# Optimization experiments

Hardware: AMD Instinct MI355X
Metric: run time of the kernel (lower is better)

Reference implementation:

```python
import jax, jax.numpy as jnp
import numpy as np
import math
from jax import lax

B, HS, WS, C, T, TD, HH, TOPM = 8, 64, 64, 512, 77, 512, 8, 3
DH = C // HH
CONF_TH = 0.35


def _layernorm(x, w, b, eps=1e-5):
    mu = x.mean(-1, keepdims=True)
    var = ((x - mu) ** 2).mean(-1, keepdims=True)
    return (x - mu) * lax.rsqrt(var + eps) * w + b


def _l2norm(x, eps=1e-6):
    n = jnp.sqrt((x * x).sum(-1, keepdims=True))
    return x / jnp.maximum(n, eps)


def _forward(visual_features, text_features, geo_mask,
             ln1_w, ln1_b, wq, bq, wk, bk, wv, bv, wo, bo,
             gate_w, gate_b, logit_scale, alpha,
             ln2_w, ln2_b, ffn_w1, ffn_b1, ffn_w2, ffn_b2):
    Bb, Hs, Ws, Cv = visual_features.shape
    N = Hs * Ws
    # Pre-LN + flatten spatial
    x = _layernorm(visual_features, ln1_w, ln1_b).reshape(Bb, N, Cv)
    q_full = x @ wq + bq                                  # [B,N,C]
    pad_mask = jnp.abs(text_features).sum(-1) <= 1e-6     # [B,T]
    k_full = text_features @ wk + bk                      # [B,T,C]
    v_full = text_features @ wv + bv
    # per-token L2 normalize over full channel dim, then split heads
    q = _l2norm(q_full).reshape(Bb, N, HH, DH)
    k = _l2norm(k_full).reshape(Bb, T, HH, DH)
    v = v_full.reshape(Bb, T, HH, DH)
    scale = jnp.exp(jnp.clip(logit_scale, -2.0, 2.0)) / jnp.sqrt(jnp.float32(DH))
    sim = jnp.einsum('bnhd,bthd->bnht', q, k) * scale     # [B,N,H,T]
    # geo gate (4D tensor branch): log-bias on logits + multiplicative channel gate later
    gate_map = jnp.clip(geo_mask, 0.3, 1.0)               # [B,1,Hs,Ws]
    geo_gate_flat = gate_map.reshape(Bb, N, 1)            # [B,N,1]
    sim = sim + jnp.log(jnp.maximum(gate_map.reshape(Bb, N), 1e-6))[:, :, None, None]
    sim = jnp.where(pad_mask[:, None, None, :], -jnp.inf, sim)
    # Top-K sparsification before softmax (threshold at the K-th value)
    topv = lax.top_k(sim, TOPM)[0]                        # [B,N,H,K]
    sim = jnp.where(sim >= topv[..., -1:], sim, -jnp.inf)
    attn = jax.nn.softmax(sim, axis=-1)
    attn = attn / jnp.maximum(attn.sum(-1, keepdims=True), 1e-6)
    # fully-padded rows -> zero
    all_pad = pad_mask.all(axis=1)
    attn = jnp.where(all_pad[:, None, None, None], 0.0, attn)
    # confidence bypass: conf = max_prob * (1 - normalized entropy), mean over heads
    a_hn = attn.transpose(0, 2, 1, 3)                     # [B,H,N,T]
    maxp = a_hn.max(-1, keepdims=True)
    t_eff = jnp.maximum((a_hn > 0).astype(a_hn.dtype).sum(-1, keepdims=True), 2.0)
    p = jnp.maximum(a_hn, 1e-8)
    ent = jnp.maximum(-(p * jnp.log(p)).sum(-1, keepdims=True) / jnp.log(t_eff), 0.0)
    conf = jnp.clip(maxp * (1.0 - ent), 0.0, 1.0).mean(axis=1)   # [B,N,1]
    conf_scale = CONF_TH + (1.0 - CONF_TH) * jnp.clip(conf, 0.0, 1.0)
    aligned = jnp.einsum('bnht,bthd->bnhd', attn, v).reshape(Bb, N, HH * DH)
    aligned = (aligned @ wo + bo) * conf_scale
    gate = jax.nn.sigmoid(x @ gate_w + gate_b) * geo_gate_flat
    y = x + alpha * gate * aligned
    h = _layernorm(y, ln2_w, ln2_b)
    y = y + (jax.nn.gelu(h @ ffn_w1 + ffn_b1, approximate=False) @ ffn_w2 + ffn_b2)
    return y.reshape(Bb, Hs, Ws, Cv)


def setup_inputs() -> dict:
    key = jax.random.key(0)
    ks = jax.random.split(key, 16)
    def w(k, shp, fan_in):
        return (jax.random.normal(k, shp, jnp.float32) * (1.0 / math.sqrt(fan_in))).astype(jnp.float32)
    return {
        'visual_features': jax.random.normal(ks[0], (B, HS, WS, C), jnp.float32),
        'text_features':   jax.random.normal(ks[1], (B, T, TD), jnp.float32),
        'geo_mask':        jax.random.uniform(ks[2], (B, 1, HS, WS), jnp.float32),
        'ln1_w': jnp.ones((C,), jnp.float32), 'ln1_b': jnp.zeros((C,), jnp.float32),
        'wq': w(ks[3], (C, C), C),   'bq': jnp.zeros((C,), jnp.float32),
        'wk': w(ks[4], (TD, C), TD), 'bk': jnp.zeros((C,), jnp.float32),
        'wv': w(ks[5], (TD, C), TD), 'bv': jnp.zeros((C,), jnp.float32),
        'wo': w(ks[6], (C, C), C),   'bo': jnp.zeros((C,), jnp.float32),
        'gate_w': w(ks[7], (C, C), C), 'gate_b': jnp.zeros((C,), jnp.float32),
        'logit_scale': jnp.float32(math.log(1.0 / 0.07)),
        'alpha': jnp.float32(0.1),
        'ln2_w': jnp.ones((C,), jnp.float32), 'ln2_b': jnp.zeros((C,), jnp.float32),
        'ffn_w1': w(ks[8], (C, 4 * C), C),    'ffn_b1': jnp.zeros((4 * C,), jnp.float32),
        'ffn_w2': w(ks[9], (4 * C, C), 4 * C), 'ffn_b2': jnp.zeros((C,), jnp.float32),
    }


def reference(visual_features, text_features, geo_mask,
              ln1_w, ln1_b, wq, bq, wk, bk, wv, bv, wo, bo,
              gate_w, gate_b, logit_scale, alpha,
              ln2_w, ln2_b, ffn_w1, ffn_b1, ffn_w2, ffn_b2):
    return _forward(visual_features, text_features, geo_mask,
                    ln1_w, ln1_b, wq, bq, wk, bk, wv, bv, wo, bo,
                    gate_w, gate_b, logit_scale, alpha,
                    ln2_w, ln2_b, ffn_w1, ffn_b1, ffn_w2, ffn_b2)
```

## Files before the change

kernel.cpp:

```cpp
#include <hip/hip_runtime.h>
#include <hip/hip_bf16.h>
#include <math.h>

#define TT 77
#define MTOT 32768

typedef __attribute__((ext_vector_type(8))) short bf16x8;
typedef __attribute__((ext_vector_type(4))) float floatx4;

#define GPTR(p) ((const __attribute__((address_space(1))) void*)(p))
#define LPTR(p) ((__attribute__((address_space(3))) void*)(p))

__device__ __forceinline__ float wred_sum(float v) {
#pragma unroll
  for (int o = 32; o >= 1; o >>= 1) v += __shfl_xor(v, o, 64);
  return v;
}

__device__ __forceinline__ unsigned short f2bf(float f) {
  unsigned int u = __float_as_uint(f);
  unsigned int r = (u + 0x7fffu + ((u >> 16) & 1u)) >> 16;
  return (unsigned short)r;
}
__device__ __forceinline__ float bf2f(unsigned short h) {
  return __uint_as_float(((unsigned int)h) << 16);
}
__device__ __forceinline__ unsigned int cvt2bf(float a, float b) {
  unsigned int r;
  asm("v_cvt_pk_bf16_f32 %0, %1, %2" : "=v"(r) : "v"(a), "v"(b));
  return r;
}

__device__ __forceinline__ float fast_gelu(float o) {
  const float z = fabsf(o) * 0.70710678118654752f;
  const float t = __builtin_amdgcn_rcpf(fmaf(0.3275911f, z, 1.0f));
  float p = fmaf(1.061405429f, t, -1.453152027f);
  p = fmaf(p, t, 1.421413741f);
  p = fmaf(p, t, -0.284496736f);
  p = fmaf(p, t, 0.254829592f);
  p = p * t;
  const float erfz = fmaf(-p, __expf(-z * z), 1.0f);
  const float s = __builtin_copysignf(erfz, o);
  return 0.5f * o * (1.0f + s);
}

__device__ __forceinline__ float fast_sigmoid(float o) {
  return __builtin_amdgcn_rcpf(1.0f + __expf(-o));
}

__global__ __launch_bounds__(256)
void ln_bf16_kernel(const float* __restrict__ in, const float* __restrict__ gw,
                    const float* __restrict__ gb, unsigned short* __restrict__ out) {
  const int wv = threadIdx.x >> 6, lane = threadIdx.x & 63;
  const size_t row = (size_t)blockIdx.x * 4 + wv;
  const float* p = in + row * 512 + lane * 8;
  float4 a = *(const float4*)p;
  float4 b = *(const float4*)(p + 4);
  float s = a.x + a.y + a.z + a.w + b.x + b.y + b.z + b.w;
  float mu = wred_sum(s) * (1.0f / 512.0f);
  float d[8] = {a.x - mu, a.y - mu, a.z - mu, a.w - mu,
                b.x - mu, b.y - mu, b.z - mu, b.w - mu};
  float ss = 0.f;
#pragma unroll
  for (int i = 0; i < 8; ++i) ss = fmaf(d[i], d[i], ss);
  float var = wred_sum(ss) * (1.0f / 512.0f);
  float rstd = rsqrtf(var + 1e-5f);
  float4 w0 = *(const float4*)(gw + lane * 8);
  float4 w1 = *(const float4*)(gw + lane * 8 + 4);
  float4 c0 = *(const float4*)(gb + lane * 8);
  float4 c1 = *(const float4*)(gb + lane * 8 + 4);
  float o[8];
  o[0] = d[0] * rstd * w0.x + c0.x;  o[1] = d[1] * rstd * w0.y + c0.y;
  o[2] = d[2] * rstd * w0.z + c0.z;  o[3] = d[3] * rstd * w0.w + c0.w;
  o[4] = d[4] * rstd * w1.x + c1.x;  o[5] = d[5] * rstd * w1.y + c1.y;
  o[6] = d[6] * rstd * w1.z + c1.z;  o[7] = d[7] * rstd * w1.w + c1.w;
  __align__(16) unsigned short ob[8];
#pragma unroll
  for (int i = 0; i < 8; ++i) ob[i] = f2bf(o[i]);
  *(uint4*)(out + row * 512 + lane * 8) = *(const uint4*)ob;
}

__global__ __launch_bounds__(256)
void zero_acc_kernel(float* __restrict__ ssq, float* __restrict__ conf) {
  const int i = blockIdx.x * 256 + threadIdx.x;
  ssq[i] = 0.0f;
  conf[i] = 0.0f;
}

__global__ __launch_bounds__(256)
void transpose_bf16_kernel(const float* __restrict__ W, unsigned short* __restrict__ WTb,
                           int K, int N) {
  __shared__ float s[32][33];
  const int tx = threadIdx.x & 31, ty = threadIdx.x >> 5;
  const int n0 = blockIdx.x * 32, k0 = blockIdx.y * 32;
#pragma unroll
  for (int j = 0; j < 4; ++j)
    s[ty + 8 * j][tx] = W[(size_t)(k0 + ty + 8 * j) * N + n0 + tx];
  __syncthreads();
#pragma unroll
  for (int j = 0; j < 4; ++j)
    WTb[(size_t)(n0 + ty + 8 * j) * K + k0 + tx] = f2bf(s[tx][ty + 8 * j]);
}

__global__ __launch_bounds__(256)
void transpose_pair_kernel(const float* __restrict__ W,
                           unsigned short* __restrict__ WTh,
                           unsigned short* __restrict__ WTl, int K, int N) {
  __shared__ float s[32][33];
  const int tx = threadIdx.x & 31, ty = threadIdx.x >> 5;
  const int n0 = blockIdx.x * 32, k0 = blockIdx.y * 32;
#pragma unroll
  for (int j = 0; j < 4; ++j)
    s[ty + 8 * j][tx] = W[(size_t)(k0 + ty + 8 * j) * N + n0 + tx];
  __syncthreads();
#pragma unroll
  for (int j = 0; j < 4; ++j) {
    const float a = s[tx][ty + 8 * j];
    const unsigned short hi = f2bf(a);
    WTh[(size_t)(n0 + ty + 8 * j) * K + k0 + tx] = hi;
    WTl[(size_t)(n0 + ty + 8 * j) * K + k0 + tx] = f2bf(a - bf2f(hi));
  }
}

__global__ __launch_bounds__(256)
void text_cvt_kernel(const float* __restrict__ text,
                     unsigned short* __restrict__ thi,
                     unsigned short* __restrict__ tlo,
                     float* __restrict__ negm) {
  const int wv = threadIdx.x >> 6, lane = threadIdx.x & 63;
  const int row = blockIdx.x * 4 + wv;
  if (row >= 616) {
    const uint4 z = {0u, 0u, 0u, 0u};
    *(uint4*)(thi + (size_t)row * 512 + lane * 8) = z;
    *(uint4*)(tlo + (size_t)row * 512 + lane * 8) = z;
    return;
  }
  const float* p = text + (size_t)row * 512 + lane * 8;
  float4 a = *(const float4*)p;
  float4 b = *(const float4*)(p + 4);
  float v[8] = {a.x, a.y, a.z, a.w, b.x, b.y, b.z, b.w};
  float ab = 0.f;
#pragma unroll
  for (int i = 0; i < 8; ++i) ab += fabsf(v[i]);
  ab = wred_sum(ab);
  __align__(16) unsigned short hb[8];
  __align__(16) unsigned short lb[8];
#pragma unroll
  for (int i = 0; i < 8; ++i) {
    hb[i] = f2bf(v[i]);
    lb[i] = f2bf(v[i] - bf2f(hb[i]));
  }
  *(uint4*)(thi + (size_t)row * 512 + lane * 8) = *(const uint4*)hb;
  *(uint4*)(tlo + (size_t)row * 512 + lane * 8) = *(const uint4*)lb;
  if (lane == 0) {
    const int bb = row / 77, t = row - bb * 77;
    negm[bb * 80 + t] = (ab <= 1e-6f) ? -INFINITY : 0.0f;
  }
}

__global__ __launch_bounds__(256)
void kv_gemm(const unsigned short* __restrict__ AH,
             const unsigned short* __restrict__ AL,
             const unsigned short* __restrict__ BH,
             const unsigned short* __restrict__ BL,
             const float* __restrict__ bk, const float* __restrict__ bv,
             float* __restrict__ outp) {
  const int K = 512;
  __shared__ __align__(16) unsigned short AsH[128 * 32];
  __shared__ __align__(16) unsigned short AsL[128 * 32];
  __shared__ __align__(16) unsigned short BsH[128 * 32];
  __shared__ __align__(16) unsigned short BsL[128 * 32];
  const int tid = threadIdx.x;
  const int wid = tid >> 6, lane = tid & 63;
  const int wr = wid >> 1, wc = wid & 1;
  const int m16 = lane & 15, quad = lane >> 4;
  const int row0 = blockIdx.y * 128, col0 = blockIdx.x * 128;

  const floatx4 zero4 = {0.f, 0.f, 0.f, 0.f};
  floatx4 acc[4][4];
#pragma unroll
  for (int i = 0; i < 4; ++i)
#pragma unroll
    for (int j = 0; j < 4; ++j) acc[i][j] = zero4;

  const int srow = tid >> 2;
  const int schunk = (tid & 3) ^ (srow & 3);
  const unsigned short* AgH = AH + (size_t)(row0 + srow) * K + schunk * 8;
  const unsigned short* AgL = AL + (size_t)(row0 + srow) * K + schunk * 8;
  const unsigned short* BgH = BH + (size_t)(col0 + srow) * K + schunk * 8;
  const unsigned short* BgL = BL + (size_t)(col0 + srow) * K + schunk * 8;
  char* AsHB = (char*)AsH + tid * 16;
  char* AsLB = (char*)AsL + tid * 16;
  char* BsHB = (char*)BsH + tid * 16;
  char* BsLB = (char*)BsL + tid * 16;
  const int rq = quad ^ (m16 & 3);
  const int aOfs = (wr * 64 + m16) * 32 + rq * 8;
  const int bOfs = (wc * 64 + m16) * 32 + rq * 8;

  for (int k0 = 0; k0 < K; k0 += 32) {
    __syncthreads();
    __builtin_amdgcn_global_load_lds(GPTR(AgH + k0), LPTR(AsHB), 16, 0, 0);
    __builtin_amdgcn_global_load_lds(GPTR(AgH + (size_t)64 * K + k0), LPTR(AsHB + 4096), 16, 0, 0);
    __builtin_amdgcn_global_load_lds(GPTR(AgL + k0), LPTR(AsLB), 16, 0, 0);
    __builtin_amdgcn_global_load_lds(GPTR(AgL + (size_t)64 * K + k0), LPTR(AsLB + 4096), 16, 0, 0);
    __builtin_amdgcn_global_load_lds(GPTR(BgH + k0), LPTR(BsHB), 16, 0, 0);
    __builtin_amdgcn_global_load_lds(GPTR(BgH + (size_t)64 * K + k0), LPTR(BsHB + 4096), 16, 0, 0);
    __builtin_amdgcn_global_load_lds(GPTR(BgL + k0), LPTR(BsLB), 16, 0, 0);
    __builtin_amdgcn_global_load_lds(GPTR(BgL + (size_t)64 * K + k0), LPTR(BsLB + 4096), 16, 0, 0);
    __syncthreads();
    bf16x8 afH[4], afL[4], bfH[4], bfL[4];
#pragma unroll
    for (int i = 0; i < 4; ++i) {
      afH[i] = *(const bf16x8*)(AsH + aOfs + i * 16 * 32);
      afL[i] = *(const bf16x8*)(AsL + aOfs + i * 16 * 32);
      bfH[i] = *(const bf16x8*)(BsH + bOfs + i * 16 * 32);
      bfL[i] = *(const bf16x8*)(BsL + bOfs + i * 16 * 32);
    }
#pragma unroll
    for (int mi = 0; mi < 4; ++mi)
#pragma unroll
      for (int ni = 0; ni < 4; ++ni) {
        acc[mi][ni] = __builtin_amdgcn_mfma_f32_16x16x32_bf16(afH[mi], bfH[ni], acc[mi][ni], 0, 0, 0);
        acc[mi][ni] = __builtin_amdgcn_mfma_f32_16x16x32_bf16(afH[mi], bfL[ni], acc[mi][ni], 0, 0, 0);
        acc[mi][ni] = __builtin_amdgcn_mfma_f32_16x16x32_bf16(afL[mi], bfH[ni], acc[mi][ni], 0, 0, 0);
      }
  }

  const float* bp = (col0 < 512) ? bk : bv;
  const int cbase = (col0 < 512) ? col0 : col0 - 512;
  float bb[4];
#pragma unroll
  for (int ni = 0; ni < 4; ++ni) bb[ni] = bp[cbase + wc * 64 + ni * 16 + m16];
#pragma unroll
  for (int mi = 0; mi < 4; ++mi)
#pragma unroll
    for (int r = 0; r < 4; ++r) {
      const int row = row0 + wr * 64 + mi * 16 + quad * 4 + r;
#pragma unroll
      for (int ni = 0; ni < 4; ++ni) {
        const int col = col0 + wc * 64 + ni * 16 + m16;
        outp[(size_t)row * 1024 + col] = acc[mi][ni][r] + bb[ni];
      }
    }
}

__global__ __launch_bounds__(256)
void knorm_kernel(const float* __restrict__ KV,
                  unsigned short* __restrict__ khb) {
  const int wv = threadIdx.x >> 6, lane = threadIdx.x & 63;
  const int row = blockIdx.x * 4 + wv;
  const float* p = KV + (size_t)row * 1024 + lane * 8;
  float4 a = *(const float4*)p;
  float4 b = *(const float4*)(p + 4);
  float v[8] = {a.x, a.y, a.z, a.w, b.x, b.y, b.z, b.w};
  float ss = 0.f;
#pragma unroll
  for (int i = 0; i < 8; ++i) ss = fmaf(v[i], v[i], ss);
  ss = wred_sum(ss);
  const float sc = 1.0f / fmaxf(sqrtf(ss), 1e-6f);
  const int bb = row / 77, t = row - bb * 77;
  const int c = lane * 8, h = c >> 6, d = c & 63;
  __align__(16) unsigned short ob[8];
#pragma unroll
  for (int i = 0; i < 8; ++i) ob[i] = f2bf(v[i] * sc);
  *(uint4*)(khb + (((size_t)bb * 8 + h) * 80 + t) * 64 + d) = *(const uint4*)ob;
}

__global__ __launch_bounds__(256)
void kpad_zero_kernel(unsigned short* __restrict__ khb, float* __restrict__ negm) {
  const int i = blockIdx.x * 256 + threadIdx.x;
  const int bh = i / 192, rem = i - bh * 192;
  const int t = 77 + rem / 64, d = rem & 63;
  khb[(((size_t)bh) * 80 + t) * 64 + d] = 0;
  if (i < 24) negm[(i / 3) * 80 + 77 + (i % 3)] = -INFINITY;
}

__global__ __launch_bounds__(256)
void sim_attn_kernel(const unsigned short* __restrict__ qnb,
                     const unsigned short* __restrict__ khb,
                     const float* __restrict__ negm,
                     const float* __restrict__ ssq,
                     const float* __restrict__ logit_scale,
                     const float* __restrict__ vf,
                     unsigned short* __restrict__ alignedb,
                     float* __restrict__ confacc) {
  __shared__ __align__(16) char lbuf[128 * 81 * 4];
  unsigned short* As = (unsigned short*)lbuf;
  unsigned short* Bs = As + 128 * 72;
  float* simt = (float*)lbuf;

  const int bh = blockIdx.y;
  const int b = bh >> 3, h = bh & 7;
  const int row0 = blockIdx.x * 128;
  const int tid = threadIdx.x;

  {
    const int r = tid >> 1, half = tid & 1;
    const unsigned short* src = qnb + ((size_t)b * 4096 + row0 + r) * 512 + h * 64 + half * 32;
    unsigned short* dst = As + r * 72 + half * 32;
    *(uint4*)dst = *(const uint4*)src;
    *(uint4*)(dst + 8) = *(const uint4*)(src + 8);
    *(uint4*)(dst + 16) = *(const uint4*)(src + 16);
    *(uint4*)(dst + 24) = *(const uint4*)(src + 24);
  }
  if (tid < 160) {
    const int r = tid >> 1, half = tid & 1;
    const unsigned short* src = khb + ((size_t)bh * 80 + r) * 64 + half * 32;
    unsigned short* dst = Bs + r * 72 + half * 32;
    *(uint4*)dst = *(const uint4*)src;
    *(uint4*)(dst + 8) = *(const uint4*)(src + 8);
    *(uint4*)(dst + 16) = *(const uint4*)(src + 16);
    *(uint4*)(dst + 24) = *(const uint4*)(src + 24);
  }
  __syncthreads();

  const int w = tid >> 6, lane = tid & 63;
  const int m16 = lane & 15, quad = lane >> 4;
  const unsigned short* aBase = As + (w * 32 + m16) * 72 + quad * 8;
  const unsigned short* bBase = Bs + m16 * 72 + quad * 8;
  bf16x8 af[2][2], bf[5][2];
#pragma unroll
  for (int mi = 0; mi < 2; ++mi)
#pragma unroll
    for (int kk = 0; kk < 2; ++kk)
      af[mi][kk] = *(const bf16x8*)(aBase + mi * 16 * 72 + kk * 32);
#pragma unroll
  for (int ni = 0; ni < 5; ++ni)
#pragma unroll
    for (int kk = 0; kk < 2; ++kk)
      bf[ni][kk] = *(const bf16x8*)(bBase + ni * 16 * 72 + kk * 32);
  __syncthreads();

  const floatx4 zero4 = {0.f, 0.f, 0.f, 0.f};
  floatx4 acc[2][5];
#pragma unroll
  for (int mi = 0; mi < 2; ++mi)
#pragma unroll
    for (int ni = 0; ni < 5; ++ni) acc[mi][ni] = zero4;
#pragma unroll
  for (int kk = 0; kk < 2; ++kk)
#pragma unroll
    for (int mi = 0; mi < 2; ++mi)
#pragma unroll
      for (int ni = 0; ni < 5; ++ni)
        acc[mi][ni] = __builtin_amdgcn_mfma_f32_16x16x32_bf16(af[mi][kk], bf[ni][kk], acc[mi][ni], 0, 0, 0);

  const float ls = fminf(fmaxf(logit_scale[0], -2.0f), 2.0f);
  const float scale = expf(ls) * 0.125f;
  float nm[5];
#pragma unroll
  for (int ni = 0; ni < 5; ++ni) nm[ni] = negm[b * 80 + ni * 16 + m16];
#pragma unroll
  for (int mi = 0; mi < 2; ++mi)
#pragma unroll
    for (int r = 0; r < 4; ++r) {
      const int lr = w * 32 + quad * 4 + mi * 16 + r;
      const float ssv = ssq[(size_t)b * 4096 + row0 + lr];
      const float nsc = scale / fmaxf(sqrtf(ssv), 1e-6f);
#pragma unroll
      for (int ni = 0; ni < 5; ++ni)
        simt[lr * 81 + ni * 16 + m16] = acc[mi][ni][r] * nsc + nm[ni];
    }
  __syncthreads();

  const int lr = tid >> 1, half = tid & 1;
  const int n = row0 + lr;
  const float* sp = simt + lr * 81;

  float m1 = -INFINITY, m2 = -INFINITY, m3 = -INFINITY, m4 = -INFINITY;
  int a1 = 0, a2 = 0, a3 = 0;
  for (int t = 0; t < 80; ++t) {
    const float v = sp[t];
    const bool c1 = v > m1, c2 = v > m2, c3 = v > m3, c4 = v > m4;
    m4 = c4 ? (c3 ? m3 : v) : m4;
    m3 = c3 ? (c2 ? m2 : v) : m3;
    a3 = c3 ? (c2 ? a2 : t) : a3;
    m2 = c2 ? (c1 ? m1 : v) : m2;
    a2 = c2 ? (c1 ? a1 : t) : a2;
    m1 = c1 ? v : m1;
    a1 = c1 ? t : a1;
  }

  const bool dead = (m1 == -INFINITY);
  if (dead) m1 = 0.0f;
  const bool tie = (!dead) && ((m1 == m2) || (m2 == m3) || (m3 == m4));

  const float d2 = m2 - m1, d3 = m3 - m1;
  const float e2 = __expf(d2), e3 = __expf(d3);
  float s0 = 1.0f + e2 + e3;
  float s1 = ((e2 > 0.f) ? e2 * d2 : 0.f) + ((e3 > 0.f) ? e3 * d3 : 0.f);
  float cntf = 1.0f + ((e2 > 0.f) ? 1.f : 0.f) + ((e3 > 0.f) ? 1.f : 0.f);

  unsigned short* op = alignedb + ((size_t)b * 4096 + n) * 512 + h * 64 + half * 32;

  if (tie) {
    s0 = 0.f; s1 = 0.f; cntf = 0.f;
    float4 acc2[8];
#pragma unroll
    for (int i = 0; i < 8; ++i) acc2[i] = (float4){0.f, 0.f, 0.f, 0.f};
    for (int t = 0; t < 80; ++t) {
      const float v = sp[t];
      if (v >= m3) {
        const float e = expf(v - m1);
        if (e > 0.f) {
          s0 += e; s1 = fmaf(e, v - m1, s1); cntf += 1.f;
          const float4* vp = (const float4*)(vf + (size_t)(b * 77 + t) * 1024 + h * 64 + half * 32);
#pragma unroll
          for (int i = 0; i < 8; ++i) {
            const float4 x = vp[i];
            acc2[i].x = fmaf(e, x.x, acc2[i].x);
            acc2[i].y = fmaf(e, x.y, acc2[i].y);
            acc2[i].z = fmaf(e, x.z, acc2[i].z);
            acc2[i].w = fmaf(e, x.w, acc2[i].w);
          }
        }
      }
    }
    const float invt = 1.0f / s0;
#pragma unroll
    for (int i = 0; i < 4; ++i) {
      const float4 lo = acc2[2 * i], hi = acc2[2 * i + 1];
      uint4 pk;
      pk.x = cvt2bf(lo.x * invt, lo.y * invt);
      pk.y = cvt2bf(lo.z * invt, lo.w * invt);
      pk.z = cvt2bf(hi.x * invt, hi.y * invt);
      pk.w = cvt2bf(hi.z * invt, hi.w * invt);
      *(uint4*)(op + i * 8) = pk;
    }
  } else {
    const float inv0 = 1.0f / s0;
    const float wA = dead ? 0.f : inv0;
    const float wB = e2 * inv0, wC = e3 * inv0;
    const float* v1p = vf + (size_t)(b * 77 + a1) * 1024 + h * 64 + half * 32;
    const float* v2p = vf + (size_t)(b * 77 + a2) * 1024 + h * 64 + half * 32;
    const float* v3p = vf + (size_t)(b * 77 + a3) * 1024 + h * 64 + half * 32;
#pragma unroll
    for (int i = 0; i < 4; ++i) {
      const float4 x0 = ((const float4*)v1p)[2 * i];
      const float4 x1 = ((const float4*)v1p)[2 * i + 1];
      const float4 y0 = ((const float4*)v2p)[2 * i];
      const float4 y1 = ((const float4*)v2p)[2 * i + 1];
      const float4 z0 = ((const float4*)v3p)[2 * i];
      const float4 z1 = ((const float4*)v3p)[2 * i + 1];
      float4 r0, r1;
      r0.x = fmaf(wC, z0.x, fmaf(wB, y0.x, wA * x0.x));
      r0.y = fmaf(wC, z0.y, fmaf(wB, y0.y, wA * x0.y));
      r0.z = fmaf(wC, z0.z, fmaf(wB, y0.z, wA * x0.z));
      r0.w = fmaf(wC, z0.w, fmaf(wB, y0.w, wA * x0.w));
      r1.x = fmaf(wC, z1.x, fmaf(wB, y1.x, wA * x1.x));
      r1.y = fmaf(wC, z1.y, fmaf(wB, y1.y, wA * x1.y));
      r1.z = fmaf(wC, z1.z, fmaf(wB, y1.z, wA * x1.z));
      r1.w = fmaf(wC, z1.w, fmaf(wB, y1.w, wA * x1.w));
      uint4 pk;
      pk.x = cvt2bf(r0.x, r0.y);
      pk.y = cvt2bf(r0.z, r0.w);
      pk.z = cvt2bf(r1.x, r1.y);
      pk.w = cvt2bf(r1.z, r1.w);
      *(uint4*)(op + i * 8) = pk;
    }
  }

  if (half == 0) {
    const float inv = 1.0f / s0;
    const float entn = (__logf(s0) - s1 * inv) + (77.0f - cntf) * 1.8420681e-7f;
    const float ent = fmaxf(entn / __logf(fmaxf(cntf, 2.0f)), 0.0f);
    float conf_h = fminf(fmaxf(inv * (1.0f - ent), 0.0f), 1.0f);
    if (dead) conf_h = 0.f;
    atomicAdd(confacc + (size_t)b * 4096 + n, conf_h * 0.125f);
  }
}

template <int EPI, int KC>
__global__ __launch_bounds__(256)
void mfma_gemm(const unsigned short* __restrict__ A,
               const unsigned short* __restrict__ WT,
               const float* __restrict__ bias,
               void* __restrict__ outv, int M, int N,
               const unsigned short* __restrict__ e0b,
               const float* __restrict__ e1f,
               const float* __restrict__ e2f,
               const float* __restrict__ scf) {
  __shared__ __align__(16) unsigned short As[128 * 64];
  __shared__ __align__(16) unsigned short Bs[128 * 64];
  const int tid = threadIdx.x;
  const int wid = tid >> 6, lane = tid & 63;
  const int wr = wid >> 1, wc = wid & 1;
  const int m16 = lane & 15, quad = lane >> 4;

  const int nwg = gridDim.x * gridDim.y;
  const int orig = blockIdx.y * gridDim.x + blockIdx.x;
  const int qq = nwg >> 3, rr = nwg & 7;
  const int xcd = orig & 7, base = orig >> 3;
  const int logical = (xcd < rr ? xcd * (qq + 1) : rr * (qq + 1) + (xcd - rr) * qq) + base;
  const int bx = logical % gridDim.x, by = logical / gridDim.x;
  const int row0 = by * 128, col0 = bx * 128;

  const floatx4 zero4 = {0.f, 0.f, 0.f, 0.f};
  floatx4 acc[4][4];
#pragma unroll
  for (int i = 0; i < 4; ++i)
#pragma unroll
    for (int j = 0; j < 4; ++j) acc[i][j] = zero4;

  size_t aoff[4], boff[4];
  char* ldst[4];
#pragma unroll
  for (int j = 0; j < 4; ++j) {
    const int s = wid * 64 + j * 256 + lane;
    const int r = s >> 3;
    const int gc = (s & 7) ^ (r & 7);
    aoff[j] = (size_t)(row0 + r) * KC + gc * 8;
    const int br = (r & 64) + 4 * (r & 15) + ((r >> 4) & 3);
    boff[j] = (size_t)(col0 + br) * KC + gc * 8;
    ldst[j] = (char*)nullptr + (size_t)s * 16;
  }

  for (int k0 = 0; k0 < KC; k0 += 64) {
    __syncthreads();
#pragma unroll
    for (int j = 0; j < 4; ++j) {
      __builtin_amdgcn_global_load_lds(GPTR(A + aoff[j] + k0), LPTR((char*)As + (size_t)(ldst[j] - (char*)nullptr)), 16, 0, 0);
      __builtin_amdgcn_global_load_lds(GPTR(WT + boff[j] + k0), LPTR((char*)Bs + (size_t)(ldst[j] - (char*)nullptr)), 16, 0, 0);
    }
    __syncthreads();
#pragma unroll
    for (int kk = 0; kk < 2; ++kk) {
      const int pc = (kk * 4 + quad) ^ (m16 & 7);
      bf16x8 af[4], bfr[4];
#pragma unroll
      for (int i = 0; i < 4; ++i) {
        af[i] = *(const bf16x8*)((const char*)As + (wr * 64 + i * 16 + m16) * 128 + pc * 16);
        bfr[i] = *(const bf16x8*)((const char*)Bs + (wc * 64 + i * 16 + m16) * 128 + pc * 16);
      }
#pragma unroll
      for (int mi = 0; mi < 4; ++mi)
#pragma unroll
        for (int ni = 0; ni < 4; ++ni)
          acc[mi][ni] = __builtin_amdgcn_mfma_f32_16x16x32_bf16(af[mi], bfr[ni], acc[mi][ni], 0, 0, 0);
    }
  }

  float* outf = (float*)outv;
  unsigned short* outb = (unsigned short*)outv;
  const unsigned short* albf = (const unsigned short*)e1f;
  const int colb = col0 + wc * 64 + 4 * m16;
  const float4 bbv = *(const float4*)(bias + colb);
  const float bb[4] = {bbv.x, bbv.y, bbv.z, bbv.w};
  const float alphav = (EPI == 2) ? scf[0] : 0.f;

#pragma unroll
  for (int mi = 0; mi < 4; ++mi) {
#pragma unroll
    for (int r = 0; r < 4; ++r) {
      const int row = row0 + wr * 64 + mi * 16 + quad * 4 + r;
      float o[4];
#pragma unroll
      for (int ni = 0; ni < 4; ++ni) o[ni] = acc[mi][ni][r] + bb[ni];
      const size_t basei = (size_t)row * N + colb;

      if (EPI == 5) {
        uint2 pk;
        pk.x = cvt2bf(o[0], o[1]);
        pk.y = cvt2bf(o[2], o[3]);
        *(uint2*)(outb + basei) = pk;
        float p = fmaf(o[0], o[0], fmaf(o[1], o[1], fmaf(o[2], o[2], o[3] * o[3])));
        p += __shfl_xor(p, 1, 64);
        p += __shfl_xor(p, 2, 64);
        p += __shfl_xor(p, 4, 64);
        p += __shfl_xor(p, 8, 64);
        if (m16 == 0) atomicAdd(const_cast<float*>(e1f) + row, p);
      } else if (EPI == 3) {
        uint2 pk;
        pk.x = cvt2bf(fast_gelu(o[0]), fast_gelu(o[1]));
        pk.y = cvt2bf(fast_gelu(o[2]), fast_gelu(o[3]));
        *(uint2*)(outb + basei) = pk;
      } else if (EPI == 1) {
        const float cm = fminf(fmaxf(e1f[row], 0.0f), 1.0f);
        const float rowscale = 0.35f + 0.65f * cm;
        uint2 pk;
        pk.x = cvt2bf(o[0] * rowscale, o[1] * rowscale);
        pk.y = cvt2bf(o[2] * rowscale, o[3] * rowscale);
        *(uint2*)(outb + basei) = pk;
      } else if (EPI == 2) {
        const float geo = fminf(fmaxf(e2f[row], 0.3f), 1.0f);
        const uint2 xpk = *(const uint2*)(e0b + basei);
        const uint2 apk = *(const uint2*)(albf + basei);
        const float xv[4] = {bf2f((unsigned short)xpk.x), bf2f((unsigned short)(xpk.x >> 16)),
                             bf2f((unsigned short)xpk.y), bf2f((unsigned short)(xpk.y >> 16))};
        const float av[4] = {bf2f((unsigned short)apk.x), bf2f((unsigned short)(apk.x >> 16)),
                             bf2f((unsigned short)apk.y), bf2f((unsigned short)(apk.y >> 16))};
        float4 ov;
        ov.x = xv[0] + alphav * fast_sigmoid(o[0]) * geo * av[0];
        ov.y = xv[1] + alphav * fast_sigmoid(o[1]) * geo * av[1];
        ov.z = xv[2] + alphav * fast_sigmoid(o[2]) * geo * av[2];
        ov.w = xv[3] + alphav * fast_sigmoid(o[3]) * geo * av[3];
        *(float4*)(outf + basei) = ov;
      } else {
        const float4 rv = *(const float4*)(e1f + basei);
        float4 ov;
        ov.x = o[0] + rv.x;
        ov.y = o[1] + rv.y;
        ov.z = o[2] + rv.z;
        ov.w = o[3] + rv.w;
        *(float4*)(outf + basei) = ov;
      }
    }
  }
}

extern "C" void kernel_launch(void* const* d_in, const int* in_sizes, int n_in,
                              void* d_out, int out_size, void* d_ws, size_t ws_size,
                              hipStream_t stream) {
  const float* visual = (const float*)d_in[0];
  const float* text   = (const float*)d_in[1];
  const float* geo    = (const float*)d_in[2];
  const float* ln1_w  = (const float*)d_in[3];
  const float* ln1_b  = (const float*)d_in[4];
  const float* wq     = (const float*)d_in[5];
  const float* bq     = (const float*)d_in[6];
  const float* wk     = (const float*)d_in[7];
  const float* bk     = (const float*)d_in[8];
  const float* wvw    = (const float*)d_in[9];
  const float* bv     = (const float*)d_in[10];
  const float* wo     = (const float*)d_in[11];
  const float* bo     = (const float*)d_in[12];
  const float* gate_w = (const float*)d_in[13];
  const float* gate_b = (const float*)d_in[14];
  const float* logit_scale = (const float*)d_in[15];
  const float* alpha  = (const float*)d_in[16];
  const float* ln2_w  = (const float*)d_in[17];
  const float* ln2_b  = (const float*)d_in[18];
  const float* ffn_w1 = (const float*)d_in[19];
  const float* ffn_b1 = (const float*)d_in[20];
  const float* ffn_w2 = (const float*)d_in[21];
  const float* ffn_b2 = (const float*)d_in[22];
  float* out = (float*)d_out;

  char* ws = (char*)d_ws;
  float* R0            = (float*)ws;
  float* BUF2          = (float*)(ws + 88080384);
  unsigned short* Xb   = (unsigned short*)(ws + 155189248);
  unsigned short* QNb  = (unsigned short*)(ws + 188743680);
  unsigned short* wqT  = (unsigned short*)(ws + 222298112);
  unsigned short* woT  = wqT + 262144;
  unsigned short* gateT = woT + 262144;
  unsigned short* w1T  = gateT + 262144;
  unsigned short* w2T  = w1T + 1048576;
  unsigned short* KHb  = w2T + 1048576;
  float* NEGM = (float*)(ws + 230146048);
  float* CONF = (float*)(ws + 230148608);
  float* SSQ  = (float*)(ws + 230279680);

  float* KV            = (float*)(ws + 88080384);
  unsigned short* THi  = (unsigned short*)(ws + 88080384 + 2621440);
  unsigned short* TLo  = THi + 640 * 512;
  unsigned short* WKVh = TLo + 640 * 512;
  unsigned short* WKVl = WKVh + 1024 * 512;

  unsigned short* ALb = (unsigned short*)R0;
  unsigned short* AOb = QNb;

  transpose_bf16_kernel<<<dim3(16, 16), 256, 0, stream>>>(wq, wqT, 512, 512);
  transpose_bf16_kernel<<<dim3(16, 16), 256, 0, stream>>>(wo, woT, 512, 512);
  transpose_bf16_kernel<<<dim3(16, 16), 256, 0, stream>>>(gate_w, gateT, 512, 512);
  transpose_bf16_kernel<<<dim3(64, 16), 256, 0, stream>>>(ffn_w1, w1T, 512, 2048);
  transpose_bf16_kernel<<<dim3(16, 64), 256, 0, stream>>>(ffn_w2, w2T, 2048, 512);
  transpose_pair_kernel<<<dim3(16, 16), 256, 0, stream>>>(wk, WKVh, WKVl, 512, 512);
  transpose_pair_kernel<<<dim3(16, 16), 256, 0, stream>>>(wvw, WKVh + 512 * 512, WKVl + 512 * 512, 512, 512);

  ln_bf16_kernel<<<MTOT / 4, 256, 0, stream>>>(visual, ln1_w, ln1_b, Xb);
  zero_acc_kernel<<<128, 256, 0, stream>>>(SSQ, CONF);
  text_cvt_kernel<<<160, 256, 0, stream>>>(text, THi, TLo, NEGM);
  kv_gemm<<<dim3(8, 5), 256, 0, stream>>>(THi, TLo, WKVh, WKVl, bk, bv, KV);
  knorm_kernel<<<154, 256, 0, stream>>>(KV, KHb);
  kpad_zero_kernel<<<48, 256, 0, stream>>>(KHb, NEGM);
  mfma_gemm<5, 512><<<dim3(4, 256), 256, 0, stream>>>(Xb, wqT, bq, QNb, MTOT, 512,
                                                      nullptr, SSQ, nullptr, nullptr);
  sim_attn_kernel<<<dim3(32, 64), 256, 0, stream>>>(QNb, KHb, NEGM, SSQ, logit_scale,
                                                    KV + 512, ALb, CONF);
  mfma_gemm<1, 512><<<dim3(4, 256), 256, 0, stream>>>(ALb, woT, bo, AOb, MTOT, 512,
                                                      nullptr, CONF, nullptr, nullptr);
  mfma_gemm<2, 512><<<dim3(4, 256), 256, 0, stream>>>(Xb, gateT, gate_b, BUF2, MTOT, 512,
                                                      Xb, (const float*)AOb, geo, alpha);
  ln_bf16_kernel<<<MTOT / 4, 256, 0, stream>>>(BUF2, ln2_w, ln2_b, Xb);
  unsigned short* GCH = (unsigned short*)R0;
  for (int ch = 0; ch < 2; ++ch) {
    const size_t off = (size_t)ch * 16384;
    mfma_gemm<3, 512><<<dim3(16, 128), 256, 0, stream>>>(Xb + off * 512, w1T, ffn_b1, GCH,
                                                         16384, 2048,
                                                         nullptr, nullptr, nullptr, nullptr);
    mfma_gemm<4, 2048><<<dim3(4, 128), 256, 0, stream>>>(GCH, w2T, ffn_b2, out + off * 512,
                                                         16384, 512,
                                                         nullptr, BUF2 + off * 512, nullptr, nullptr);
  }
}
```

Measured before the change: 567.6 us.

## Double-buffer LDS tiles in MFMA GEMM to overlap global loads with compute

```diff
diff --git a/kernel.cpp b/kernel.cpp
--- a/kernel.cpp
+++ b/kernel.cpp
@@ -480,8 +480,8 @@
                const float* __restrict__ e1f,
                const float* __restrict__ e2f,
                const float* __restrict__ scf) {
-  __shared__ __align__(16) unsigned short As[128 * 64];
-  __shared__ __align__(16) unsigned short Bs[128 * 64];
+  __shared__ __align__(16) unsigned short As[2][128 * 64];
+  __shared__ __align__(16) unsigned short Bs[2][128 * 64];
   const int tid = threadIdx.x;
   const int wid = tid >> 6, lane = tid & 63;
   const int wr = wid >> 1, wc = wid & 1;
@@ -503,7 +503,7 @@
     for (int j = 0; j < 4; ++j) acc[i][j] = zero4;
 
   size_t aoff[4], boff[4];
-  char* ldst[4];
+  unsigned int ldso[4];
 #pragma unroll
   for (int j = 0; j < 4; ++j) {
     const int s = wid * 64 + j * 256 + lane;
@@ -512,31 +512,45 @@
     aoff[j] = (size_t)(row0 + r) * KC + gc * 8;
     const int br = (r & 64) + 4 * (r & 15) + ((r >> 4) & 3);
     boff[j] = (size_t)(col0 + br) * KC + gc * 8;
-    ldst[j] = (char*)nullptr + (size_t)s * 16;
-  }
-
-  for (int k0 = 0; k0 < KC; k0 += 64) {
-    __syncthreads();
-#pragma unroll
-    for (int j = 0; j < 4; ++j) {
-      __builtin_amdgcn_global_load_lds(GPTR(A + aoff[j] + k0), LPTR((char*)As + (size_t)(ldst[j] - (char*)nullptr)), 16, 0, 0);
-      __builtin_amdgcn_global_load_lds(GPTR(WT + boff[j] + k0), LPTR((char*)Bs + (size_t)(ldst[j] - (char*)nullptr)), 16, 0, 0);
-    }
-    __syncthreads();
+    ldso[j] = (unsigned int)s * 16;
+  }
+
+  constexpr int NT = KC / 64;
+#pragma unroll
+  for (int j = 0; j < 4; ++j) {
+    __builtin_amdgcn_global_load_lds(GPTR(A + aoff[j]), LPTR((char*)As[0] + ldso[j]), 16, 0, 0);
+    __builtin_amdgcn_global_load_lds(GPTR(WT + boff[j]), LPTR((char*)Bs[0] + ldso[j]), 16, 0, 0);
+  }
+  __syncthreads();
+
+  int cur = 0;
+  for (int t = 0; t < NT; ++t) {
+    if (t + 1 < NT) {
+      const size_t k0n = (size_t)(t + 1) * 64;
+#pragma unroll
+      for (int j = 0; j < 4; ++j) {
+        __builtin_amdgcn_global_load_lds(GPTR(A + aoff[j] + k0n), LPTR((char*)As[cur ^ 1] + ldso[j]), 16, 0, 0);
+        __builtin_amdgcn_global_load_lds(GPTR(WT + boff[j] + k0n), LPTR((char*)Bs[cur ^ 1] + ldso[j]), 16, 0, 0);
+      }
+    }
 #pragma unroll
     for (int kk = 0; kk < 2; ++kk) {
       const int pc = (kk * 4 + quad) ^ (m16 & 7);
       bf16x8 af[4], bfr[4];
 #pragma unroll
       for (int i = 0; i < 4; ++i) {
-        af[i] = *(const bf16x8*)((const char*)As + (wr * 64 + i * 16 + m16) * 128 + pc * 16);
-        bfr[i] = *(const bf16x8*)((const char*)Bs + (wc * 64 + i * 16 + m16) * 128 + pc * 16);
+        af[i] = *(const bf16x8*)((const char*)As[cur] + (wr * 64 + i * 16 + m16) * 128 + pc * 16);
+        bfr[i] = *(const bf16x8*)((const char*)Bs[cur] + (wc * 64 + i * 16 + m16) * 128 + pc * 16);
       }
 #pragma unroll
       for (int mi = 0; mi < 4; ++mi)
 #pragma unroll
         for (int ni = 0; ni < 4; ++ni)
           acc[mi][ni] = __builtin_amdgcn_mfma_f32_16x16x32_bf16(af[mi], bfr[ni], acc[mi][ni], 0, 0, 0);
+    }
+    if (t + 1 < NT) {
+      __syncthreads();
+      cur ^= 1;
     }
   }
 
```

Measured after the change: 625.1 us. 1.1x slower.
